# Kernel optimization log

Measured on AMD Instinct MI355X. Metric: run time of the kernel, lower is better.

Reference implementation:

```python
import jax, jax.numpy as jnp
from jax import lax
import numpy as np

H = 64  # hidden size

def lstm_layer(x, w_ih, w_hh, b_ih, b_hh):
    # x: [B,T,I]; w_ih: [4H,I]; w_hh: [4H,H]; gates ordered i,f,g,o (PyTorch)
    B = x.shape[0]
    xg = jnp.einsum('bti,gi->btg', x, w_ih) + b_ih  # precompute input projections [B,T,4H]
    h0 = jnp.zeros((B, H), x.dtype)
    c0 = jnp.zeros((B, H), x.dtype)
    def step(carry, xt):
        h, c = carry
        gates = xt + h @ w_hh.T + b_hh
        i, f, g, o = jnp.split(gates, 4, axis=-1)
        c = jax.nn.sigmoid(f) * c + jax.nn.sigmoid(i) * jnp.tanh(g)
        h = jax.nn.sigmoid(o) * jnp.tanh(c)
        return (h, c), h
    (hT, cT), hs = lax.scan(step, (h0, c0), jnp.swapaxes(xg, 0, 1))
    return jnp.swapaxes(hs, 0, 1), hT, cT

def layernorm(x, g, b, eps=1e-5):
    mu = jnp.mean(x, axis=-1, keepdims=True)
    var = jnp.mean(jnp.square(x - mu), axis=-1, keepdims=True)
    return (x - mu) * lax.rsqrt(var + eps) * g + b

def setup_inputs() -> dict:
    key = jax.random.key(0)
    ks = jax.random.split(key, 16)
    s = 0.05
    return {
        'x': jax.random.normal(ks[0], (512, 1024, 32), jnp.float32),
        'w_ih1': jax.random.normal(ks[1], (4 * H, 32)) * s,
        'w_hh1': jax.random.normal(ks[2], (4 * H, H)) * s,
        'b_ih1': jax.random.normal(ks[3], (4 * H,)) * s,
        'b_hh1': jax.random.normal(ks[4], (4 * H,)) * s,
        'w_ih2': jax.random.normal(ks[5], (4 * H, H)) * s,
        'w_hh2': jax.random.normal(ks[6], (4 * H, H)) * s,
        'b_ih2': jax.random.normal(ks[7], (4 * H,)) * s,
        'b_hh2': jax.random.normal(ks[8], (4 * H,)) * s,
        'fc1_w': jax.random.normal(ks[9], (128, H)) * s,
        'fc1_b': jax.random.normal(ks[10], (128,)) * s,
        'fc2_w': jax.random.normal(ks[11], (128, 128)) * s,
        'fc2_b': jax.random.normal(ks[12], (128,)) * s,
        'ln_g': jnp.ones((128,), jnp.float32),
        'ln_b': jnp.zeros((128,), jnp.float32),
    }

def reference(x, w_ih1, w_hh1, b_ih1, b_hh1, w_ih2, w_hh2, b_ih2, b_hh2,
              fc1_w, fc1_b, fc2_w, fc2_b, ln_g, ln_b):
    h1, _, _ = lstm_layer(x, w_ih1, w_hh1, b_ih1, b_hh1)
    # dropout(0.1) is identity in eval mode
    _, hT, _ = lstm_layer(h1, w_ih2, w_hh2, b_ih2, b_hh2)
    y = jax.nn.relu(hT @ fc1_w.T + fc1_b)
    y = y @ fc2_w.T + fc2_b
    return layernorm(y, ln_g, ln_b)
```

## Files before the change

kernel.cpp:

```cpp
#include <hip/hip_runtime.h>
#include <cstdint>
#include <cstddef>

#define T_STEPS 1024
#define SEG     8
#define NSEG    (T_STEPS / SEG)
#define NBLK    256
#define LOG2E   1.4426950408889634f
#define UPERM(k, c) ((((c) << 1) + ((k) & 1)) + (((k) >> 1) << 5))

typedef __attribute__((ext_vector_type(8))) _Float16 half8;
typedef __attribute__((ext_vector_type(4))) float    f32x4;
typedef __attribute__((ext_vector_type(4))) int      i32x4;

static __device__ __forceinline__ float fexp2(float x) {
#if defined(__has_builtin) && __has_builtin(__builtin_amdgcn_exp2f)
  return __builtin_amdgcn_exp2f(x);
#else
  return __exp2f(x);
#endif
}
static __device__ __forceinline__ float sigm2(float a) {
  return __builtin_amdgcn_rcpf(1.0f + fexp2(-a));
}
static __device__ __forceinline__ float tanhg2(float a) {
  return 2.0f * __builtin_amdgcn_rcpf(1.0f + fexp2(-(a + a))) - 1.0f;
}
static __device__ __forceinline__ float tanhc(float c) {
  return 1.0f - 2.0f * __builtin_amdgcn_rcpf(1.0f + fexp2(c * (2.0f * LOG2E)));
}

static __device__ __forceinline__ half8 load8s(const float* s, float sc) {
  float4 a = ((const float4*)s)[0];
  float4 b = ((const float4*)s)[1];
  half8 h;
  h[0] = (_Float16)(a.x * sc); h[1] = (_Float16)(a.y * sc);
  h[2] = (_Float16)(a.z * sc); h[3] = (_Float16)(a.w * sc);
  h[4] = (_Float16)(b.x * sc); h[5] = (_Float16)(b.y * sc);
  h[6] = (_Float16)(b.z * sc); h[7] = (_Float16)(b.w * sc);
  return h;
}
static __device__ __forceinline__ i32x4 quant16(const float* src, float s) {
  union { i32x4 v; signed char b[16]; } u;
  #pragma unroll
  for (int j = 0; j < 16; ++j) u.b[j] = (signed char)__float2int_rn(src[j] * s);
  return u.v;
}

static __device__ __forceinline__ void barrier_lds() {
  __asm__ volatile("s_waitcnt lgkmcnt(0)\n\ts_barrier" ::: "memory");
}

__global__ __launch_bounds__(256, 1) void lstm_fused(
    const float* __restrict__ x,
    const float* __restrict__ w_ih1, const float* __restrict__ w_hh1,
    const float* __restrict__ b_ih1, const float* __restrict__ b_hh1,
    const float* __restrict__ w_ih2, const float* __restrict__ w_hh2,
    const float* __restrict__ b_ih2, const float* __restrict__ b_hh2,
    const float* __restrict__ fc1_w, const float* __restrict__ fc1_b,
    const float* __restrict__ fc2_w, const float* __restrict__ fc2_b,
    const float* __restrict__ ln_g, const float* __restrict__ ln_b,
    float* __restrict__ out)
{
  __shared__ __align__(16) signed char h1ring[32][2][64];
  __shared__ __align__(16) signed char h2ring[2][2][64];
  __shared__ __align__(16) float xg1b[2][SEG][2][64][4];
  __shared__ __align__(16) float xg2b[2][SEG][2][64][4];
  __shared__ __align__(16) float hfin[2][64];
  __shared__ __align__(16) float y1s[2][128];
  __shared__ __align__(16) float y2s[2][128];
  __shared__ float redmu[2], redrs[2];

  const int t   = threadIdx.x;
  const int blk = blockIdx.x;
  const int l   = t & 63;
  const int w   = t >> 6;
  const int col = l & 15;
  const int q   = l >> 4;

  {
    int* hp = (int*)h1ring;
    #pragma unroll
    for (int i = 0; i < 4; ++i) hp[t + i * 256] = 0;
    if (t < 64) ((int*)h2ring)[t] = 0;
  }

  const i32x4 zi = (i32x4){0, 0, 0, 0};
  f32x4 zf; zf[0] = 0.f; zf[1] = 0.f; zf[2] = 0.f; zf[3] = 0.f;

  i32x4 wq[4][4];
  half8 wbx[4][4];
  f32x4 fsa0, fsa1;
  float fsx[4][4];
  float bL[4][4];

  if (w < 3) {
    const float* W = (w == 0) ? w_hh1 : (w == 1) ? w_hh2 : w_ih2;
    float fs[4][4];
    #pragma unroll
    for (int g = 0; g < 4; ++g) {
      #pragma unroll
      for (int k = 0; k < 4; ++k) {
        const int r = g * 64 + UPERM(k, col);
        const float* p = W + r * 64 + q * 16;
        float m = 0.0f;
        #pragma unroll
        for (int j = 0; j < 16; ++j) m = fmaxf(m, fabsf(p[j]));
        m = fmaxf(m, __shfl_xor(m, 16, 64));
        m = fmaxf(m, __shfl_xor(m, 32, 64));
        wq[g][k] = quant16(p, 127.0f / m);
        fs[g][k] = m * (LOG2E / 16129.0f);
      }
    }
    if (w == 2) {
      #pragma unroll
      for (int g = 0; g < 4; ++g) {
        #pragma unroll
        for (int k = 0; k < 4; ++k) {
          const int r = g * 64 + UPERM(k, col);
          fsx[g][k] = fs[g][k];
          bL[g][k]  = (b_ih2[r] + b_hh2[r]) * LOG2E;
        }
      }
    } else if (l & 32) {
      fsa0[0] = fs[0][2]; fsa0[1] = fs[1][2]; fsa0[2] = fs[2][2]; fsa0[3] = fs[3][2];
      fsa1[0] = fs[0][3]; fsa1[1] = fs[1][3]; fsa1[2] = fs[2][3]; fsa1[3] = fs[3][3];
    } else {
      fsa0[0] = fs[0][0]; fsa0[1] = fs[1][0]; fsa0[2] = fs[2][0]; fsa0[3] = fs[3][0];
      fsa1[0] = fs[0][1]; fsa1[1] = fs[1][1]; fsa1[2] = fs[2][1]; fsa1[3] = fs[3][1];
    }
  } else {
    #pragma unroll
    for (int g = 0; g < 4; ++g) {
      #pragma unroll
      for (int k = 0; k < 4; ++k) {
        const int r = g * 64 + UPERM(k, col);
        wbx[g][k] = load8s(w_ih1 + r * 32 + q * 8, LOG2E);
        bL[g][k]  = (b_ih1[r] + b_hh1[r]) * LOG2E;
      }
    }
  }

  const int ab    = q & 1;
  const int u0    = ((l & 15) << 1) + ((l >> 5) << 5);
  const int bfrag = ((l & 15) >> 2) & 1;
  const int hi    = l & 32;
  const int arow  = (l & 15) >> 1;
  const int axb   = l & 1;

  float c0 = 0.0f, c1 = 0.0f;

  auto produce_xg1 = [&](int tau) {
    const float* xs = x + ((size_t)(2 * blk + axb) * T_STEPS + (tau * SEG + arow)) * 32 + q * 8;
    const float4 va = ((const float4*)xs)[0];
    const float4 vb = ((const float4*)xs)[1];
    half8 xf;
    xf[0] = (_Float16)va.x; xf[1] = (_Float16)va.y;
    xf[2] = (_Float16)va.z; xf[3] = (_Float16)va.w;
    xf[4] = (_Float16)vb.x; xf[5] = (_Float16)vb.y;
    xf[6] = (_Float16)vb.z; xf[7] = (_Float16)vb.w;
    f32x4 accf[4][4];
    #pragma unroll
    for (int g = 0; g < 4; ++g)
      #pragma unroll
      for (int k = 0; k < 4; ++k)
        accf[g][k] = __builtin_amdgcn_mfma_f32_16x16x32_f16(xf, wbx[g][k], zf, 0, 0, 0);
    float* dst = &xg1b[tau & 1][0][0][0][0];
    #pragma unroll
    for (int k = 0; k < 4; ++k) {
      #pragma unroll
      for (int r = 0; r < 4; ++r) {
        const int row = q * 4 + r;
        f32x4 v;
        v[0] = accf[0][k][r] + bL[0][k];
        v[1] = accf[1][k][r] + bL[1][k];
        v[2] = accf[2][k][r] + bL[2][k];
        v[3] = accf[3][k][r] + bL[3][k];
        *(f32x4*)(dst + (size_t)(row * 64 + UPERM(k, col)) * 4) = v;
      }
    }
  };

  auto produce_xg2 = [&](int sg) {
    const i32x4 a = *(const i32x4*)((const signed char*)h1ring +
                    (size_t)((((sg * SEG + arow) & 31) * 128) + axb * 64 + q * 16));
    i32x4 acc[4][4];
    #pragma unroll
    for (int g = 0; g < 4; ++g)
      #pragma unroll
      for (int k = 0; k < 4; ++k)
        acc[g][k] = __builtin_amdgcn_mfma_i32_16x16x64_i8(a, wq[g][k], zi, 0, 0, 0);
    float* dst = &xg2b[sg & 1][0][0][0][0];
    #pragma unroll
    for (int k = 0; k < 4; ++k) {
      #pragma unroll
      for (int r = 0; r < 4; ++r) {
        const int row = q * 4 + r;
        f32x4 v;
        v[0] = bL[0][k] + fsx[0][k] * (float)acc[0][k][r];
        v[1] = bL[1][k] + fsx[1][k] * (float)acc[1][k][r];
        v[2] = bL[2][k] + fsx[2][k] * (float)acc[2][k][r];
        v[3] = bL[3][k] + fsx[3][k] * (float)acc[3][k][r];
        *(f32x4*)(dst + (size_t)(row * 64 + UPERM(k, col)) * 4) = v;
      }
    }
  };

  auto run_seg = [&](const float* XG, signed char* RING, int RM, int t0, int isl2) {
    #pragma unroll
    for (int j8 = 0; j8 < SEG; ++j8) {
      const int tt = t0 + j8;
      const i32x4 a = *(const i32x4*)(RING + ((tt - 1) & RM) * 128 + bfrag * 64 + q * 16);
      const f32x4 xv0 = *(const f32x4*)(XG + (size_t)((j8 * 2 + ab) * 64 + u0) * 4);
      const f32x4 xv1 = *(const f32x4*)(XG + (size_t)((j8 * 2 + ab) * 64 + u0 + 1) * 4);
      i32x4 acc[4][4];
      #pragma unroll
      for (int g = 0; g < 4; ++g)
        #pragma unroll
        for (int k = 0; k < 4; ++k)
          acc[g][k] = __builtin_amdgcn_mfma_i32_16x16x64_i8(a, wq[g][k], zi, 0, 0, 0);
      const int i00 = hi ? acc[0][2][0] : acc[0][0][0];
      const int i01 = hi ? acc[1][2][0] : acc[1][0][0];
      const int i02 = hi ? acc[2][2][0] : acc[2][0][0];
      const int i03 = hi ? acc[3][2][0] : acc[3][0][0];
      const float p00 = xv0[0] + fsa0[0] * (float)i00;
      const float p01 = xv0[1] + fsa0[1] * (float)i01;
      const float p02 = xv0[2] + fsa0[2] * (float)i02;
      const float p03 = xv0[3] + fsa0[3] * (float)i03;
      const float gi0 = sigm2(p00), gf0 = sigm2(p01);
      const float gg0 = tanhg2(p02), go0 = sigm2(p03);
      c0 = gf0 * c0 + gi0 * gg0;
      const float h0 = go0 * tanhc(c0);
      const int i10 = hi ? acc[0][3][0] : acc[0][1][0];
      const int i11 = hi ? acc[1][3][0] : acc[1][1][0];
      const int i12 = hi ? acc[2][3][0] : acc[2][1][0];
      const int i13 = hi ? acc[3][3][0] : acc[3][1][0];
      const float p10 = xv1[0] + fsa1[0] * (float)i10;
      const float p11 = xv1[1] + fsa1[1] * (float)i11;
      const float p12 = xv1[2] + fsa1[2] * (float)i12;
      const float p13 = xv1[3] + fsa1[3] * (float)i13;
      const float gi1 = sigm2(p10), gf1 = sigm2(p11);
      const float gg1 = tanhg2(p12), go1 = sigm2(p13);
      c1 = gf1 * c1 + gi1 * gg1;
      const float h1v = go1 * tanhc(c1);
      signed char* wp = RING + (tt & RM) * 128 + ab * 64 + u0;
      wp[0] = (signed char)__float2int_rn(h0  * 127.0f);
      wp[1] = (signed char)__float2int_rn(h1v * 127.0f);
      if (isl2 && tt == T_STEPS - 1) {
        hfin[ab][u0]     = h0;
        hfin[ab][u0 + 1] = h1v;
      }
    }
  };

  if (w == 3) produce_xg1(0);
  barrier_lds();

  for (int s = 0; s <= NSEG + 1; ++s) {
    if (w == 0) {
      if (s < NSEG)
        run_seg(&xg1b[s & 1][0][0][0][0], (signed char*)h1ring, 31, s * SEG, 0);
    } else if (w == 1) {
      const int sg = s - 2;
      if (sg >= 0)
        run_seg(&xg2b[sg & 1][0][0][0][0], (signed char*)h2ring, 1, sg * SEG, 1);
    } else if (w == 2) {
      const int sg = s - 1;
      if (sg >= 0 && sg < NSEG) produce_xg2(sg);
    } else {
      if (s + 1 < NSEG) produce_xg1(s + 1);
    }
    barrier_lds();
  }

  __syncthreads();

  if (t < 256) {
    const int bi = t >> 7, j = t & 127;
    float accv = fc1_b[j];
    const float4* w4 = (const float4*)(fc1_w + j * 64);
    const float4* h4 = (const float4*)hfin[bi];
    #pragma unroll
    for (int qq = 0; qq < 16; ++qq) {
      float4 wv = w4[qq]; float4 hv = h4[qq];
      accv += wv.x * hv.x + wv.y * hv.y + wv.z * hv.z + wv.w * hv.w;
    }
    y1s[bi][j] = fmaxf(accv, 0.0f);
  }
  __syncthreads();
  if (t < 256) {
    const int bi = t >> 7, j = t & 127;
    float accv = fc2_b[j];
    const float4* w4 = (const float4*)(fc2_w + j * 128);
    const float4* y4 = (const float4*)y1s[bi];
    #pragma unroll
    for (int qq = 0; qq < 32; ++qq) {
      float4 wv = w4[qq]; float4 yv = y4[qq];
      accv += wv.x * yv.x + wv.y * yv.y + wv.z * yv.z + wv.w * yv.w;
    }
    y2s[bi][j] = accv;
  }
  __syncthreads();
  if (t < 128) {
    const int bi = t >> 6, jj = t & 63;
    float s  = y2s[bi][jj] + y2s[bi][64 + jj];
    float qs = y2s[bi][jj] * y2s[bi][jj] + y2s[bi][64 + jj] * y2s[bi][64 + jj];
    #pragma unroll
    for (int off = 32; off > 0; off >>= 1) {
      s  += __shfl_down(s, off, 64);
      qs += __shfl_down(qs, off, 64);
    }
    if (jj == 0) {
      const float mu  = s * (1.0f / 128.0f);
      const float var = qs * (1.0f / 128.0f) - mu * mu;
      redmu[bi] = mu;
      redrs[bi] = rsqrtf(var + 1e-5f);
    }
  }
  __syncthreads();
  if (t < 256) {
    const int bi = t >> 7, j = t & 127;
    out[(size_t)(2 * blk + bi) * 128 + j] =
        (y2s[bi][j] - redmu[bi]) * redrs[bi] * ln_g[j] + ln_b[j];
  }
}

extern "C" void kernel_launch(void* const* d_in, const int* in_sizes, int n_in,
                              void* d_out, int out_size, void* d_ws, size_t ws_size,
                              hipStream_t stream) {
  const float* x     = (const float*)d_in[0];
  const float* w_ih1 = (const float*)d_in[1];
  const float* w_hh1 = (const float*)d_in[2];
  const float* b_ih1 = (const float*)d_in[3];
  const float* b_hh1 = (const float*)d_in[4];
  const float* w_ih2 = (const float*)d_in[5];
  const float* w_hh2 = (const float*)d_in[6];
  const float* b_ih2 = (const float*)d_in[7];
  const float* b_hh2 = (const float*)d_in[8];
  const float* fc1_w = (const float*)d_in[9];
  const float* fc1_b = (const float*)d_in[10];
  const float* fc2_w = (const float*)d_in[11];
  const float* fc2_b = (const float*)d_in[12];
  const float* ln_g  = (const float*)d_in[13];
  const float* ln_b  = (const float*)d_in[14];
  float* out = (float*)d_out;

  lstm_fused<<<NBLK, 256, 0, stream>>>(x, w_ih1, w_hh1, b_ih1, b_hh1,
                                       w_ih2, w_hh2, b_ih2, b_hh2,
                                       fc1_w, fc1_b, fc2_w, fc2_b,
                                       ln_g, ln_b, out);
}
```

Baseline: 480.2 us.

## Double warps per block: one wave per batch row in recurrence and split producers

Blocks grow from 256 to 512 threads. Each LSTM recurrence layer now uses two wavefronts, one per batch element, each handling a single hidden unit per lane instead of two, and the input-projection producers split their gate columns across two waves. The aim is to halve the serial per-step gate math on the critical recurrence path and to spread producer MFMA work. It also raises recurrence waves' priority with s_setprio. In exchange, each recurrence wave still issues the full 16 MFMAs per step and selects its lane's result, which doubles MFMA issue per CU and raises register pressure under the 512-thread launch bound.

```diff
diff --git a/kernel.cpp b/kernel.cpp
--- a/kernel.cpp
+++ b/kernel.cpp
@@ -7,7 +7,6 @@
 #define NSEG    (T_STEPS / SEG)
 #define NBLK    256
 #define LOG2E   1.4426950408889634f
-#define UPERM(k, c) ((((c) << 1) + ((k) & 1)) + (((k) >> 1) << 5))
 
 typedef __attribute__((ext_vector_type(8))) _Float16 half8;
 typedef __attribute__((ext_vector_type(4))) float    f32x4;
@@ -51,7 +50,7 @@
   __asm__ volatile("s_waitcnt lgkmcnt(0)\n\ts_barrier" ::: "memory");
 }
 
-__global__ __launch_bounds__(256, 1) void lstm_fused(
+__global__ __launch_bounds__(512, 2) void lstm_fused(
     const float* __restrict__ x,
     const float* __restrict__ w_ih1, const float* __restrict__ w_hh1,
     const float* __restrict__ b_ih1, const float* __restrict__ b_hh1,
@@ -77,31 +76,31 @@
   const int w   = t >> 6;
   const int col = l & 15;
   const int q   = l >> 4;
-
-  {
-    int* hp = (int*)h1ring;
-    #pragma unroll
-    for (int i = 0; i < 4; ++i) hp[t + i * 256] = 0;
-    if (t < 64) ((int*)h2ring)[t] = 0;
-  }
+  const int myb = w & 1;
+  const int kbase = (w & 1) * 2;
+
+  ((int*)h1ring)[t]       = 0;
+  ((int*)h1ring)[t + 512] = 0;
+  if (t < 64) ((int*)h2ring)[t] = 0;
 
   const i32x4 zi = (i32x4){0, 0, 0, 0};
   f32x4 zf; zf[0] = 0.f; zf[1] = 0.f; zf[2] = 0.f; zf[3] = 0.f;
 
   i32x4 wq[4][4];
-  half8 wbx[4][4];
-  f32x4 fsa0, fsa1;
-  float fsx[4][4];
-  float bL[4][4];
-
-  if (w < 3) {
-    const float* W = (w == 0) ? w_hh1 : (w == 1) ? w_hh2 : w_ih2;
-    float fs[4][4];
+  i32x4 wq2[4][2];
+  half8 wbx[4][2];
+  f32x4 fsa;
+  float fsx[4][2];
+  float bL[4][2];
+
+  if (w < 4) {
+    const float* W = (w < 2) ? w_hh1 : w_hh2;
+    float fsq[4][4];
     #pragma unroll
     for (int g = 0; g < 4; ++g) {
       #pragma unroll
       for (int k = 0; k < 4; ++k) {
-        const int r = g * 64 + UPERM(k, col);
+        const int r = g * 64 + k * 16 + col;
         const float* p = W + r * 64 + q * 16;
         float m = 0.0f;
         #pragma unroll
@@ -109,49 +108,51 @@
         m = fmaxf(m, __shfl_xor(m, 16, 64));
         m = fmaxf(m, __shfl_xor(m, 32, 64));
         wq[g][k] = quant16(p, 127.0f / m);
-        fs[g][k] = m * (LOG2E / 16129.0f);
-      }
-    }
-    if (w == 2) {
-      #pragma unroll
-      for (int g = 0; g < 4; ++g) {
+        fsq[g][k] = m * (LOG2E / 16129.0f);
+      }
+    }
+    #pragma unroll
+    for (int g = 0; g < 4; ++g) {
+      const float v01 = (q & 1) ? fsq[g][1] : fsq[g][0];
+      const float v23 = (q & 1) ? fsq[g][3] : fsq[g][2];
+      fsa[g] = (q & 2) ? v23 : v01;
+    }
+  } else if (w < 6) {
+    #pragma unroll
+    for (int g = 0; g < 4; ++g) {
+      #pragma unroll
+      for (int k2 = 0; k2 < 2; ++k2) {
+        const int r = g * 64 + (kbase + k2) * 16 + col;
+        const float* p = w_ih2 + r * 64 + q * 16;
+        float m = 0.0f;
         #pragma unroll
-        for (int k = 0; k < 4; ++k) {
-          const int r = g * 64 + UPERM(k, col);
-          fsx[g][k] = fs[g][k];
-          bL[g][k]  = (b_ih2[r] + b_hh2[r]) * LOG2E;
-        }
-      }
-    } else if (l & 32) {
-      fsa0[0] = fs[0][2]; fsa0[1] = fs[1][2]; fsa0[2] = fs[2][2]; fsa0[3] = fs[3][2];
-      fsa1[0] = fs[0][3]; fsa1[1] = fs[1][3]; fsa1[2] = fs[2][3]; fsa1[3] = fs[3][3];
-    } else {
-      fsa0[0] = fs[0][0]; fsa0[1] = fs[1][0]; fsa0[2] = fs[2][0]; fsa0[3] = fs[3][0];
-      fsa1[0] = fs[0][1]; fsa1[1] = fs[1][1]; fsa1[2] = fs[2][1]; fsa1[3] = fs[3][1];
+        for (int j = 0; j < 16; ++j) m = fmaxf(m, fabsf(p[j]));
+        m = fmaxf(m, __shfl_xor(m, 16, 64));
+        m = fmaxf(m, __shfl_xor(m, 32, 64));
+        wq2[g][k2] = quant16(p, 127.0f / m);
+        fsx[g][k2] = m * (LOG2E / 16129.0f);
+        bL[g][k2]  = (b_ih2[r] + b_hh2[r]) * LOG2E;
+      }
     }
   } else {
     #pragma unroll
     for (int g = 0; g < 4; ++g) {
       #pragma unroll
-      for (int k = 0; k < 4; ++k) {
-        const int r = g * 64 + UPERM(k, col);
-        wbx[g][k] = load8s(w_ih1 + r * 32 + q * 8, LOG2E);
-        bL[g][k]  = (b_ih1[r] + b_hh1[r]) * LOG2E;
-      }
-    }
-  }
-
-  const int ab    = q & 1;
-  const int u0    = ((l & 15) << 1) + ((l >> 5) << 5);
-  const int bfrag = ((l & 15) >> 2) & 1;
-  const int hi    = l & 32;
-  const int arow  = (l & 15) >> 1;
-  const int axb   = l & 1;
-
-  float c0 = 0.0f, c1 = 0.0f;
+      for (int k2 = 0; k2 < 2; ++k2) {
+        const int r = g * 64 + (kbase + k2) * 16 + col;
+        wbx[g][k2] = load8s(w_ih1 + r * 32 + q * 8, LOG2E);
+        bL[g][k2]  = (b_ih1[r] + b_hh1[r]) * LOG2E;
+      }
+    }
+  }
+
+  const int tl  = (l & 15) >> 1;
+  const int axb = l & 1;
+
+  float c = 0.0f;
 
   auto produce_xg1 = [&](int tau) {
-    const float* xs = x + ((size_t)(2 * blk + axb) * T_STEPS + (tau * SEG + arow)) * 32 + q * 8;
+    const float* xs = x + ((size_t)(2 * blk + axb) * T_STEPS + (tau * SEG + tl)) * 32 + q * 8;
     const float4 va = ((const float4*)xs)[0];
     const float4 vb = ((const float4*)xs)[1];
     half8 xf;
@@ -159,112 +160,96 @@
     xf[2] = (_Float16)va.z; xf[3] = (_Float16)va.w;
     xf[4] = (_Float16)vb.x; xf[5] = (_Float16)vb.y;
     xf[6] = (_Float16)vb.z; xf[7] = (_Float16)vb.w;
-    f32x4 accf[4][4];
+    f32x4 accf[4][2];
     #pragma unroll
     for (int g = 0; g < 4; ++g)
       #pragma unroll
-      for (int k = 0; k < 4; ++k)
-        accf[g][k] = __builtin_amdgcn_mfma_f32_16x16x32_f16(xf, wbx[g][k], zf, 0, 0, 0);
+      for (int k2 = 0; k2 < 2; ++k2)
+        accf[g][k2] = __builtin_amdgcn_mfma_f32_16x16x32_f16(xf, wbx[g][k2], zf, 0, 0, 0);
     float* dst = &xg1b[tau & 1][0][0][0][0];
     #pragma unroll
-    for (int k = 0; k < 4; ++k) {
+    for (int k2 = 0; k2 < 2; ++k2) {
       #pragma unroll
       for (int r = 0; r < 4; ++r) {
         const int row = q * 4 + r;
         f32x4 v;
-        v[0] = accf[0][k][r] + bL[0][k];
-        v[1] = accf[1][k][r] + bL[1][k];
-        v[2] = accf[2][k][r] + bL[2][k];
-        v[3] = accf[3][k][r] + bL[3][k];
-        *(f32x4*)(dst + (size_t)(row * 64 + UPERM(k, col)) * 4) = v;
+        v[0] = accf[0][k2][r] + bL[0][k2];
+        v[1] = accf[1][k2][r] + bL[1][k2];
+        v[2] = accf[2][k2][r] + bL[2][k2];
+        v[3] = accf[3][k2][r] + bL[3][k2];
+        *(f32x4*)(dst + (size_t)(row * 64 + (kbase + k2) * 16 + col) * 4) = v;
       }
     }
   };
 
   auto produce_xg2 = [&](int sg) {
     const i32x4 a = *(const i32x4*)((const signed char*)h1ring +
-                    (size_t)((((sg * SEG + arow) & 31) * 128) + axb * 64 + q * 16));
-    i32x4 acc[4][4];
+                    (size_t)((((sg * SEG + tl) & 31) * 128) + axb * 64 + q * 16));
+    i32x4 acc[4][2];
     #pragma unroll
     for (int g = 0; g < 4; ++g)
       #pragma unroll
-      for (int k = 0; k < 4; ++k)
-        acc[g][k] = __builtin_amdgcn_mfma_i32_16x16x64_i8(a, wq[g][k], zi, 0, 0, 0);
+      for (int k2 = 0; k2 < 2; ++k2)
+        acc[g][k2] = __builtin_amdgcn_mfma_i32_16x16x64_i8(a, wq2[g][k2], zi, 0, 0, 0);
     float* dst = &xg2b[sg & 1][0][0][0][0];
     #pragma unroll
-    for (int k = 0; k < 4; ++k) {
+    for (int k2 = 0; k2 < 2; ++k2) {
       #pragma unroll
       for (int r = 0; r < 4; ++r) {
         const int row = q * 4 + r;
         f32x4 v;
-        v[0] = bL[0][k] + fsx[0][k] * (float)acc[0][k][r];
-        v[1] = bL[1][k] + fsx[1][k] * (float)acc[1][k][r];
-        v[2] = bL[2][k] + fsx[2][k] * (float)acc[2][k][r];
-        v[3] = bL[3][k] + fsx[3][k] * (float)acc[3][k][r];
-        *(f32x4*)(dst + (size_t)(row * 64 + UPERM(k, col)) * 4) = v;
+        v[0] = bL[0][k2] + fsx[0][k2] * (float)acc[0][k2][r];
+        v[1] = bL[1][k2] + fsx[1][k2] * (float)acc[1][k2][r];
+        v[2] = bL[2][k2] + fsx[2][k2] * (float)acc[2][k2][r];
+        v[3] = bL[3][k2] + fsx[3][k2] * (float)acc[3][k2][r];
+        *(f32x4*)(dst + (size_t)(row * 64 + (kbase + k2) * 16 + col) * 4) = v;
       }
     }
   };
 
   auto run_seg = [&](const float* XG, signed char* RING, int RM, int t0, int isl2) {
+    __builtin_amdgcn_s_setprio(1);
     #pragma unroll
     for (int j8 = 0; j8 < SEG; ++j8) {
       const int tt = t0 + j8;
-      const i32x4 a = *(const i32x4*)(RING + ((tt - 1) & RM) * 128 + bfrag * 64 + q * 16);
-      const f32x4 xv0 = *(const f32x4*)(XG + (size_t)((j8 * 2 + ab) * 64 + u0) * 4);
-      const f32x4 xv1 = *(const f32x4*)(XG + (size_t)((j8 * 2 + ab) * 64 + u0 + 1) * 4);
+      const i32x4 a = *(const i32x4*)(RING + ((tt - 1) & RM) * 128 + myb * 64 + q * 16);
+      const f32x4 xv = *(const f32x4*)(XG + (size_t)((j8 * 2 + myb) * 64 + l) * 4);
       i32x4 acc[4][4];
       #pragma unroll
       for (int g = 0; g < 4; ++g)
         #pragma unroll
         for (int k = 0; k < 4; ++k)
           acc[g][k] = __builtin_amdgcn_mfma_i32_16x16x64_i8(a, wq[g][k], zi, 0, 0, 0);
-      const int i00 = hi ? acc[0][2][0] : acc[0][0][0];
-      const int i01 = hi ? acc[1][2][0] : acc[1][0][0];
-      const int i02 = hi ? acc[2][2][0] : acc[2][0][0];
-      const int i03 = hi ? acc[3][2][0] : acc[3][0][0];
-      const float p00 = xv0[0] + fsa0[0] * (float)i00;
-      const float p01 = xv0[1] + fsa0[1] * (float)i01;
-      const float p02 = xv0[2] + fsa0[2] * (float)i02;
-      const float p03 = xv0[3] + fsa0[3] * (float)i03;
-      const float gi0 = sigm2(p00), gf0 = sigm2(p01);
-      const float gg0 = tanhg2(p02), go0 = sigm2(p03);
-      c0 = gf0 * c0 + gi0 * gg0;
-      const float h0 = go0 * tanhc(c0);
-      const int i10 = hi ? acc[0][3][0] : acc[0][1][0];
-      const int i11 = hi ? acc[1][3][0] : acc[1][1][0];
-      const int i12 = hi ? acc[2][3][0] : acc[2][1][0];
-      const int i13 = hi ? acc[3][3][0] : acc[3][1][0];
-      const float p10 = xv1[0] + fsa1[0] * (float)i10;
-      const float p11 = xv1[1] + fsa1[1] * (float)i11;
-      const float p12 = xv1[2] + fsa1[2] * (float)i12;
-      const float p13 = xv1[3] + fsa1[3] * (float)i13;
-      const float gi1 = sigm2(p10), gf1 = sigm2(p11);
-      const float gg1 = tanhg2(p12), go1 = sigm2(p13);
-      c1 = gf1 * c1 + gi1 * gg1;
-      const float h1v = go1 * tanhc(c1);
-      signed char* wp = RING + (tt & RM) * 128 + ab * 64 + u0;
-      wp[0] = (signed char)__float2int_rn(h0  * 127.0f);
-      wp[1] = (signed char)__float2int_rn(h1v * 127.0f);
-      if (isl2 && tt == T_STEPS - 1) {
-        hfin[ab][u0]     = h0;
-        hfin[ab][u0 + 1] = h1v;
-      }
-    }
+      float p[4];
+      #pragma unroll
+      for (int g = 0; g < 4; ++g) {
+        const int v01 = (q & 1) ? acc[g][1][0] : acc[g][0][0];
+        const int v23 = (q & 1) ? acc[g][3][0] : acc[g][2][0];
+        const int ai  = (q & 2) ? v23 : v01;
+        p[g] = xv[g] + fsa[g] * (float)ai;
+      }
+      const float gi = sigm2(p[0]), gf = sigm2(p[1]);
+      const float gg = tanhg2(p[2]), go = sigm2(p[3]);
+      c = gf * c + gi * gg;
+      const float hv = go * tanhc(c);
+      RING[(tt & RM) * 128 + myb * 64 + l] = (signed char)__float2int_rn(hv * 127.0f);
+      if (isl2 && tt == T_STEPS - 1) hfin[myb][l] = hv;
+    }
+    __builtin_amdgcn_s_setprio(0);
   };
 
-  if (w == 3) produce_xg1(0);
+  if (w >= 6) produce_xg1(0);
   barrier_lds();
 
   for (int s = 0; s <= NSEG + 1; ++s) {
-    if (w == 0) {
+    if (w < 2) {
       if (s < NSEG)
         run_seg(&xg1b[s & 1][0][0][0][0], (signed char*)h1ring, 31, s * SEG, 0);
-    } else if (w == 1) {
+    } else if (w < 4) {
       const int sg = s - 2;
       if (sg >= 0)
         run_seg(&xg2b[sg & 1][0][0][0][0], (signed char*)h2ring, 1, sg * SEG, 1);
-    } else if (w == 2) {
+    } else if (w < 6) {
       const int sg = s - 1;
       if (sg >= 0 && sg < NSEG) produce_xg2(sg);
     } else {
@@ -345,7 +330,7 @@
   const float* ln_b  = (const float*)d_in[14];
   float* out = (float*)d_out;
 
-  lstm_fused<<<NBLK, 256, 0, stream>>>(x, w_ih1, w_hh1, b_ih1, b_hh1,
+  lstm_fused<<<NBLK, 512, 0, stream>>>(x, w_ih1, w_hh1, b_ih1, b_hh1,
                                        w_ih2, w_hh2, b_ih2, b_hh2,
                                        fc1_w, fc1_b, fc2_w, fc2_b,
                                        ln_g, ln_b, out);
```

Measured after the change: 409.7 us. -14.7%, faster.
